# Kernel tuning notes

Hardware: AMD Instinct MI355X
Metric: run time of the kernel (lower is better)

The kernel has to match this reference:

```python
import jax, jax.numpy as jnp
import numpy as np

R, K, H_IN, W_IN = 512, 17, 56, 56   # rois, keypoints, heatmap size
ROI_H = ROI_W = 96                   # = ceil(BOX_LEN), fixed by construction
BOX_LEN = 95.5                       # all boxes have this side length
A = -0.75                            # PyTorch bicubic coefficient


def _cubic(x):
    x = jnp.abs(x)
    near = ((A + 2.0) * x - (A + 3.0)) * x * x + 1.0
    far = A * (((x - 5.0) * x + 8.0) * x - 4.0)
    return jnp.where(x <= 1.0, near, jnp.where(x < 2.0, far, 0.0))


def _resize_matrix(out_size, in_size):
    """Dense [out,in] bicubic interpolation matrix (align_corners=False, border-replicate)."""
    scale = in_size / out_size
    src = (jnp.arange(out_size, dtype=jnp.float32) + 0.5) * scale - 0.5
    base = jnp.floor(src).astype(jnp.int32)
    taps = base[:, None] + jnp.arange(-1, 3)                      # [out, 4]
    w = _cubic(src[:, None] - taps.astype(jnp.float32))           # weights from unclamped dist
    taps = jnp.clip(taps, 0, in_size - 1)                         # replicate border
    rows = jnp.broadcast_to(jnp.arange(out_size)[:, None], taps.shape)
    return jnp.zeros((out_size, in_size), jnp.float32).at[rows, taps].add(w)


def setup_inputs() -> dict:
    key = jax.random.key(0)
    k1, k2 = jax.random.split(key)
    masks = jax.random.normal(k1, (R, K, H_IN, W_IN), dtype=jnp.float32)
    offs = jax.random.uniform(k2, (R, 2), jnp.float32, 0.0, 400.0)
    # corner format (c0_start, c1_start, c0_end, c1_end); all lengths == BOX_LEN
    boxes = jnp.concatenate([offs, offs + BOX_LEN], axis=1)
    return {"masks": masks, "boxes": boxes}


def reference(masks, boxes):
    My = _resize_matrix(ROI_H, H_IN)   # [ROI_H, H_IN]
    Mx = _resize_matrix(ROI_W, W_IN)   # [ROI_W, W_IN]
    # separable bicubic resize of every ROI heatmap: [R,K,ROI_H,ROI_W]
    roi = jnp.einsum('hi,rkij,wj->rkhw', My, masks, Mx)
    flat = roi.reshape(R, K, ROI_H * ROI_W)
    pos = jnp.argmax(flat, axis=-1)                                # [R,K]
    y = pos // ROI_W
    x = pos % ROI_W
    scores = jnp.take_along_axis(flat, pos[..., None], axis=-1)[..., 0]  # logit at argmax
    len0 = jnp.maximum(boxes[:, 2] - boxes[:, 0], 1.0)
    len1 = jnp.maximum(boxes[:, 3] - boxes[:, 1], 1.0)
    corr0 = (len0 / ROI_H)[:, None]
    corr1 = (len1 / ROI_W)[:, None]
    p0 = (y.astype(jnp.float32) + 0.5) * corr0 + boxes[:, 0:1]
    p1 = (x.astype(jnp.float32) + 0.5) * corr1 + boxes[:, 1:2]
    predictions = jnp.stack([p0, p1, jnp.ones_like(p0)], axis=1)   # [R, n_dim+1, K]
    return predictions, scores
```

## Files before the change

kernel.cpp:

```cpp
#include <hip/hip_runtime.h>

#define R_    512
#define K_    17
#define HIN   56
#define WIN   56
#define OUTS  96
#define NMAP  (R_ * K_)
#define NT    64
#define GRID  (NMAP / 2)
#define WST   18
#define TROWS 60

typedef float v2f __attribute__((ext_vector_type(2)));

#define LDS_FENCE() do {                                      \
        __builtin_amdgcn_sched_barrier(0);                    \
        asm volatile("s_waitcnt lgkmcnt(0)" ::: "memory");    \
        __builtin_amdgcn_sched_barrier(0);                    \
    } while (0)

constexpr float cubic_c(float xin) {
    float x = xin < 0.0f ? -xin : xin;
    const float A = -0.75f;
    if (x <= 1.0f) return ((A + 2.0f) * x - (A + 3.0f)) * x * x + 1.0f;
    if (x < 2.0f)  return A * (((x - 5.0f) * x + 8.0f) * x - 4.0f);
    return 0.0f;
}

struct XTabT {
    float w[OUTS][4];
    int   s[OUTS];
    constexpr XTabT() : w{}, s{} {
        for (int o = 0; o < OUTS; ++o) {
            float src = ((float)o + 0.5f) * (56.0f / 96.0f) - 0.5f;
            int base = (int)src;
            if ((float)base > src) --base;
            int st = base - 1;
            if (st < 0) st = 0;
            if (st > HIN - 4) st = HIN - 4;
            s[o] = st;
            for (int q = 0; q < 4; ++q) {
                int tap = base - 1 + q;
                float wt = cubic_c(src - (float)tap);
                int p = tap < 0 ? 0 : (tap > HIN - 1 ? HIN - 1 : tap);
                w[o][p - st] += wt;
            }
        }
    }
};
constexpr XTabT XT;

struct YTabT {
    float w[12][4];
    int   d[12];
    constexpr YTabT() : w{}, d{} {
        for (int ph = 0; ph < 12; ++ph) {
            float src = ((float)ph + 0.5f) * (56.0f / 96.0f) - 0.5f;
            int base = (int)src;
            if ((float)base > src) --base;
            d[ph] = base - 1;
            for (int q = 0; q < 4; ++q)
                w[ph][q] = cubic_c(src - (float)(base - 1 + q));
        }
    }
};
constexpr YTabT YT;

template<int G> struct FSv {
    static constexpr int v = (G == 0) ? 0 : (G == 1) ? 1 : (G == 2) ? 4
                           : (G == 3) ? 6 : (G == 4) ? 8 : 10;
};

__device__ __forceinline__ v2f yv(const v2f* c, int hh) {
    const int ph = hh % 12, bb = hh / 12;
    const int i0 = 7 * bb + YT.d[ph] + 2;
    v2f acc = c[i0] * (v2f){YT.w[ph][0], YT.w[ph][0]};
    acc = __builtin_elementwise_fma((v2f){YT.w[ph][1], YT.w[ph][1]}, c[i0 + 1], acc);
    acc = __builtin_elementwise_fma((v2f){YT.w[ph][2], YT.w[ph][2]}, c[i0 + 2], acc);
    acc = __builtin_elementwise_fma((v2f){YT.w[ph][3], YT.w[ph][3]}, c[i0 + 3], acc);
    return acc;
}

template<int G>
__device__ __forceinline__ void strip_comp(float4 a0, float4 a1, float4 a2, float4 a3,
                                           float4 b0, float4 b1, float4 b2, float4 b3,
                                           v2f* wrow,
                                           const v2f* crd,
                                           int pbase,
                                           float& m0, int& p0, float& m1, int& p1) {
    constexpr int FS = FSv<G>::v;
    v2f rr[16];
    rr[0]  = (v2f){a0.x, b0.x}; rr[1]  = (v2f){a0.y, b0.y};
    rr[2]  = (v2f){a0.z, b0.z}; rr[3]  = (v2f){a0.w, b0.w};
    rr[4]  = (v2f){a1.x, b1.x}; rr[5]  = (v2f){a1.y, b1.y};
    rr[6]  = (v2f){a1.z, b1.z}; rr[7]  = (v2f){a1.w, b1.w};
    rr[8]  = (v2f){a2.x, b2.x}; rr[9]  = (v2f){a2.y, b2.y};
    rr[10] = (v2f){a2.z, b2.z}; rr[11] = (v2f){a2.w, b2.w};
    rr[12] = (v2f){a3.x, b3.x}; rr[13] = (v2f){a3.y, b3.y};
    rr[14] = (v2f){a3.z, b3.z}; rr[15] = (v2f){a3.w, b3.w};

    LDS_FENCE();
#pragma unroll
    for (int i = 0; i < 8; ++i) {
        const int o0 = 16 * G + 2 * i, o1 = o0 + 1;
        const int s0 = XT.s[o0] - 4 * FS, s1 = XT.s[o1] - 4 * FS;
        v2f x0 = rr[s0] * (v2f){XT.w[o0][0], XT.w[o0][0]};
        x0 = __builtin_elementwise_fma((v2f){XT.w[o0][1], XT.w[o0][1]}, rr[s0 + 1], x0);
        x0 = __builtin_elementwise_fma((v2f){XT.w[o0][2], XT.w[o0][2]}, rr[s0 + 2], x0);
        x0 = __builtin_elementwise_fma((v2f){XT.w[o0][3], XT.w[o0][3]}, rr[s0 + 3], x0);
        v2f x1 = rr[s1] * (v2f){XT.w[o1][0], XT.w[o1][0]};
        x1 = __builtin_elementwise_fma((v2f){XT.w[o1][1], XT.w[o1][1]}, rr[s1 + 1], x1);
        x1 = __builtin_elementwise_fma((v2f){XT.w[o1][2], XT.w[o1][2]}, rr[s1 + 2], x1);
        x1 = __builtin_elementwise_fma((v2f){XT.w[o1][3], XT.w[o1][3]}, rr[s1 + 3], x1);
        float4 st = {x0.x, x0.y, x1.x, x1.y};
        *(float4*)(wrow + 2 * i) = st;
    }
    LDS_FENCE();

    v2f c[18];
#pragma unroll
    for (int i = 0; i < 18; ++i) c[i] = crd[i * WST];

    v2f sv = {-INFINITY, -INFINITY};
    int h0i = 0, h1i = 0;
#pragma unroll
    for (int hh = 0; hh < 24; ++hh) {
        v2f a = yv(c, hh);
        if (a.x > sv.x) { sv.x = a.x; h0i = hh; }
        if (a.y > sv.y) { sv.y = a.y; h1i = hh; }
    }
    const int fp0 = pbase + 16 * G + h0i * 96;
    const int fp1 = pbase + 16 * G + h1i * 96;
    if (sv.x > m0 || (sv.x == m0 && fp0 < p0)) { m0 = sv.x; p0 = fp0; }
    if (sv.y > m1 || (sv.y == m1 && fp1 < p1)) { m1 = sv.y; p1 = fp1; }
}

__global__ __launch_bounds__(NT)
void _Keypointer_kernel(const float* __restrict__ masks,
                        const float* __restrict__ boxes,
                        float* __restrict__ out) {
    __shared__ __align__(16) v2f tmp[TROWS * WST];

    const int w   = threadIdx.x;
    const int bm0 = 2 * blockIdx.x;

    const int srcrow = min(max(w - 2, 0), HIN - 1);
    const int phys   = min(w, TROWS - 1);
    const float* r0 = masks + (size_t)bm0 * (HIN * WIN) + srcrow * WIN;
    const float* r1 = r0 + HIN * WIN;
    v2f* wrow = tmp + phys * WST;

    const int cc = w & 15, q = w >> 4;
    const v2f* crd = tmp + (14 * q) * WST + cc;
    const int pbase = (24 * q) * OUTS + cc;

    float m0 = -INFINITY, m1 = -INFINITY;
    int   p0 = 0x7fffffff, p1 = 0x7fffffff;

    float4 A0, A1, A2, A3, B0, B1, B2, B3;
    float4 C0, C1, C2, C3, D0, D1, D2, D3;

#define LOADS(FS_, X0, X1, X2, X3, Y0, Y1, Y2, Y3) {            \
        const float4* _A = (const float4*)r0 + (FS_);           \
        const float4* _B = (const float4*)r1 + (FS_);           \
        X0 = _A[0]; X1 = _A[1]; X2 = _A[2]; X3 = _A[3];         \
        Y0 = _B[0]; Y1 = _B[1]; Y2 = _B[2]; Y3 = _B[3]; }

    LOADS(0,  A0, A1, A2, A3, B0, B1, B2, B3)
    LOADS(1,  C0, C1, C2, C3, D0, D1, D2, D3)
    strip_comp<0>(A0, A1, A2, A3, B0, B1, B2, B3, wrow, crd, pbase, m0, p0, m1, p1);
    LOADS(4,  A0, A1, A2, A3, B0, B1, B2, B3)
    strip_comp<1>(C0, C1, C2, C3, D0, D1, D2, D3, wrow, crd, pbase, m0, p0, m1, p1);
    LOADS(6,  C0, C1, C2, C3, D0, D1, D2, D3)
    strip_comp<2>(A0, A1, A2, A3, B0, B1, B2, B3, wrow, crd, pbase, m0, p0, m1, p1);
    LOADS(8,  A0, A1, A2, A3, B0, B1, B2, B3)
    strip_comp<3>(C0, C1, C2, C3, D0, D1, D2, D3, wrow, crd, pbase, m0, p0, m1, p1);
    LOADS(10, C0, C1, C2, C3, D0, D1, D2, D3)
    strip_comp<4>(A0, A1, A2, A3, B0, B1, B2, B3, wrow, crd, pbase, m0, p0, m1, p1);
    strip_comp<5>(C0, C1, C2, C3, D0, D1, D2, D3, wrow, crd, pbase, m0, p0, m1, p1);
#undef LOADS

#pragma unroll
    for (int off = 32; off; off >>= 1) {
        float t0 = __shfl_xor(m0, off, 64); int u0 = __shfl_xor(p0, off, 64);
        if (t0 > m0 || (t0 == m0 && u0 < p0)) { m0 = t0; p0 = u0; }
        float t1 = __shfl_xor(m1, off, 64); int u1 = __shfl_xor(p1, off, 64);
        if (t1 > m1 || (t1 == m1 && u1 < p1)) { m1 = t1; p1 = u1; }
    }

    if (w == 0) {
#pragma unroll
        for (int mi = 0; mi < 2; ++mi) {
            const int map = bm0 + mi;
            const float M = mi ? m1 : m0;
            const int bp  = mi ? p1 : p0;
            const int r = map / K_, k = map - r * K_;
            const int y = bp / OUTS, x = bp - y * OUTS;
            const float b0f = boxes[r * 4 + 0], b1f = boxes[r * 4 + 1];
            const float b2f = boxes[r * 4 + 2], b3f = boxes[r * 4 + 3];
            const float corr0 = fmaxf(b2f - b0f, 1.0f) / (float)OUTS;
            const float corr1 = fmaxf(b3f - b1f, 1.0f) / (float)OUTS;
            const float pp0 = ((float)y + 0.5f) * corr0 + b0f;
            const float pp1 = ((float)x + 0.5f) * corr1 + b1f;
            out[(r * 3 + 0) * K_ + k] = pp0;
            out[(r * 3 + 1) * K_ + k] = pp1;
            out[(r * 3 + 2) * K_ + k] = 1.0f;
            out[R_ * 3 * K_ + r * K_ + k] = M;
        }
    }
}

extern "C" void kernel_launch(void* const* d_in, const int* in_sizes, int n_in,
                              void* d_out, int out_size, void* d_ws, size_t ws_size,
                              hipStream_t stream) {
    const float* masks = (const float*)d_in[0];
    const float* boxes = (const float*)d_in[1];
    float* out = (float*)d_out;
    _Keypointer_kernel<<<GRID, NT, 0, stream>>>(masks, boxes, out);
}
```

Measured before the change: 180.8 us.

## Restructure into persistent 384-thread blocks with LDS-staged, double-buffered map pairs

The kernel moves from one 64-thread wave per map pair to persistent 384-thread blocks that each handle four map pairs. Each pair's raw inputs are loaded with coalesced float4 reads and staged in LDS, and the next pair is prefetched into registers while the current one is computed. The six waves split the horizontal pass by column strip and the vertical pass by output column, then combine their argmax results through shared memory. This aims to improve load coalescing and hide global latency, at the cost of more LDS, extra __syncthreads, and fewer, larger blocks.

```diff
diff --git a/kernel.cpp b/kernel.cpp
--- a/kernel.cpp
+++ b/kernel.cpp
@@ -6,18 +6,15 @@
 #define WIN   56
 #define OUTS  96
 #define NMAP  (R_ * K_)
-#define NT    64
-#define GRID  (NMAP / 2)
-#define WST   18
+#define NT    384
+#define GRID  1088
+#define ITERS 4
+#define RST   98
 #define TROWS 60
+#define RAWST 58
+#define RAWMAP (HIN * RAWST)
 
 typedef float v2f __attribute__((ext_vector_type(2)));
-
-#define LDS_FENCE() do {                                      \
-        __builtin_amdgcn_sched_barrier(0);                    \
-        asm volatile("s_waitcnt lgkmcnt(0)" ::: "memory");    \
-        __builtin_amdgcn_sched_barrier(0);                    \
-    } while (0)
 
 constexpr float cubic_c(float xin) {
     float x = xin < 0.0f ? -xin : xin;
@@ -82,24 +79,16 @@
 }
 
 template<int G>
-__device__ __forceinline__ void strip_comp(float4 a0, float4 a1, float4 a2, float4 a3,
-                                           float4 b0, float4 b1, float4 b2, float4 b3,
-                                           v2f* wrow,
-                                           const v2f* crd,
-                                           int pbase,
-                                           float& m0, int& p0, float& m1, int& p1) {
+__device__ __forceinline__ void p1_lds(const float* rA, const float* rB, v2f* dst) {
     constexpr int FS = FSv<G>::v;
     v2f rr[16];
-    rr[0]  = (v2f){a0.x, b0.x}; rr[1]  = (v2f){a0.y, b0.y};
-    rr[2]  = (v2f){a0.z, b0.z}; rr[3]  = (v2f){a0.w, b0.w};
-    rr[4]  = (v2f){a1.x, b1.x}; rr[5]  = (v2f){a1.y, b1.y};
-    rr[6]  = (v2f){a1.z, b1.z}; rr[7]  = (v2f){a1.w, b1.w};
-    rr[8]  = (v2f){a2.x, b2.x}; rr[9]  = (v2f){a2.y, b2.y};
-    rr[10] = (v2f){a2.z, b2.z}; rr[11] = (v2f){a2.w, b2.w};
-    rr[12] = (v2f){a3.x, b3.x}; rr[13] = (v2f){a3.y, b3.y};
-    rr[14] = (v2f){a3.z, b3.z}; rr[15] = (v2f){a3.w, b3.w};
-
-    LDS_FENCE();
+#pragma unroll
+    for (int k = 0; k < 8; ++k) {
+        v2f a = *(const v2f*)(rA + 4 * FS + 2 * k);
+        v2f b = *(const v2f*)(rB + 4 * FS + 2 * k);
+        rr[2 * k]     = (v2f){a.x, b.x};
+        rr[2 * k + 1] = (v2f){a.y, b.y};
+    }
 #pragma unroll
     for (int i = 0; i < 8; ++i) {
         const int o0 = 16 * G + 2 * i, o1 = o0 + 1;
@@ -113,101 +102,125 @@
         x1 = __builtin_elementwise_fma((v2f){XT.w[o1][2], XT.w[o1][2]}, rr[s1 + 2], x1);
         x1 = __builtin_elementwise_fma((v2f){XT.w[o1][3], XT.w[o1][3]}, rr[s1 + 3], x1);
         float4 st = {x0.x, x0.y, x1.x, x1.y};
-        *(float4*)(wrow + 2 * i) = st;
-    }
-    LDS_FENCE();
-
-    v2f c[18];
-#pragma unroll
-    for (int i = 0; i < 18; ++i) c[i] = crd[i * WST];
-
-    v2f sv = {-INFINITY, -INFINITY};
-    int h0i = 0, h1i = 0;
-#pragma unroll
-    for (int hh = 0; hh < 24; ++hh) {
-        v2f a = yv(c, hh);
-        if (a.x > sv.x) { sv.x = a.x; h0i = hh; }
-        if (a.y > sv.y) { sv.y = a.y; h1i = hh; }
-    }
-    const int fp0 = pbase + 16 * G + h0i * 96;
-    const int fp1 = pbase + 16 * G + h1i * 96;
-    if (sv.x > m0 || (sv.x == m0 && fp0 < p0)) { m0 = sv.x; p0 = fp0; }
-    if (sv.y > m1 || (sv.y == m1 && fp1 < p1)) { m1 = sv.y; p1 = fp1; }
-}
-
-__global__ __launch_bounds__(NT)
+        *(float4*)(dst + 2 * i) = st;
+    }
+}
+
+__global__ __launch_bounds__(NT, 3)
 void _Keypointer_kernel(const float* __restrict__ masks,
                         const float* __restrict__ boxes,
                         float* __restrict__ out) {
-    __shared__ __align__(16) v2f tmp[TROWS * WST];
-
-    const int w   = threadIdx.x;
-    const int bm0 = 2 * blockIdx.x;
+    __shared__ float raw[2 * RAWMAP];
+    __shared__ __align__(16) v2f tmp[TROWS * RST];
+    __shared__ v2f wvmax[6];
+    __shared__ int wppos[6][2];
+
+    const int t = threadIdx.x;
+    const int g = t >> 6;
+    const int w = t & 63;
+
+    int off0, off1, off2, off3, off4;
+#define MKOFF(f_, dst_) { const int f = (f_); const int mp = (f >= 784);          \
+        const int rem = f - 784 * mp; const int row = rem / 14;                   \
+        const int c4 = rem - 14 * row; dst_ = mp * RAWMAP + row * RAWST + 4 * c4; }
+    MKOFF(t,        off0) MKOFF(t + 384,  off1)
+    MKOFF(t + 768,  off2) MKOFF(t + 1152, off3)
+    MKOFF(1536 + (t & 31), off4)
+#undef MKOFF
 
     const int srcrow = min(max(w - 2, 0), HIN - 1);
     const int phys   = min(w, TROWS - 1);
-    const float* r0 = masks + (size_t)bm0 * (HIN * WIN) + srcrow * WIN;
-    const float* r1 = r0 + HIN * WIN;
-    v2f* wrow = tmp + phys * WST;
-
-    const int cc = w & 15, q = w >> 4;
-    const v2f* crd = tmp + (14 * q) * WST + cc;
-    const int pbase = (24 * q) * OUTS + cc;
-
-    float m0 = -INFINITY, m1 = -INFINITY;
-    int   p0 = 0x7fffffff, p1 = 0x7fffffff;
-
-    float4 A0, A1, A2, A3, B0, B1, B2, B3;
-    float4 C0, C1, C2, C3, D0, D1, D2, D3;
-
-#define LOADS(FS_, X0, X1, X2, X3, Y0, Y1, Y2, Y3) {            \
-        const float4* _A = (const float4*)r0 + (FS_);           \
-        const float4* _B = (const float4*)r1 + (FS_);           \
-        X0 = _A[0]; X1 = _A[1]; X2 = _A[2]; X3 = _A[3];         \
-        Y0 = _B[0]; Y1 = _B[1]; Y2 = _B[2]; Y3 = _B[3]; }
-
-    LOADS(0,  A0, A1, A2, A3, B0, B1, B2, B3)
-    LOADS(1,  C0, C1, C2, C3, D0, D1, D2, D3)
-    strip_comp<0>(A0, A1, A2, A3, B0, B1, B2, B3, wrow, crd, pbase, m0, p0, m1, p1);
-    LOADS(4,  A0, A1, A2, A3, B0, B1, B2, B3)
-    strip_comp<1>(C0, C1, C2, C3, D0, D1, D2, D3, wrow, crd, pbase, m0, p0, m1, p1);
-    LOADS(6,  C0, C1, C2, C3, D0, D1, D2, D3)
-    strip_comp<2>(A0, A1, A2, A3, B0, B1, B2, B3, wrow, crd, pbase, m0, p0, m1, p1);
-    LOADS(8,  A0, A1, A2, A3, B0, B1, B2, B3)
-    strip_comp<3>(C0, C1, C2, C3, D0, D1, D2, D3, wrow, crd, pbase, m0, p0, m1, p1);
-    LOADS(10, C0, C1, C2, C3, D0, D1, D2, D3)
-    strip_comp<4>(A0, A1, A2, A3, B0, B1, B2, B3, wrow, crd, pbase, m0, p0, m1, p1);
-    strip_comp<5>(C0, C1, C2, C3, D0, D1, D2, D3, wrow, crd, pbase, m0, p0, m1, p1);
-#undef LOADS
-
-#pragma unroll
-    for (int off = 32; off; off >>= 1) {
-        float t0 = __shfl_xor(m0, off, 64); int u0 = __shfl_xor(p0, off, 64);
-        if (t0 > m0 || (t0 == m0 && u0 < p0)) { m0 = t0; p0 = u0; }
-        float t1 = __shfl_xor(m1, off, 64); int u1 = __shfl_xor(p1, off, 64);
-        if (t1 > m1 || (t1 == m1 && u1 < p1)) { m1 = t1; p1 = u1; }
-    }
-
-    if (w == 0) {
-#pragma unroll
-        for (int mi = 0; mi < 2; ++mi) {
-            const int map = bm0 + mi;
-            const float M = mi ? m1 : m0;
-            const int bp  = mi ? p1 : p0;
+    v2f* dst = tmp + phys * RST + 16 * g;
+    const float* rA = raw + srcrow * RAWST;
+    const float* rB = rA + RAWMAP;
+
+    const int q   = t / 96;
+    const int col = t - 96 * q;
+    const int h0  = 24 * q;
+    const v2f* crd = tmp + (14 * q) * RST + col;
+
+    float4 V0, V1, V2, V3, V4;
+
+    int pair = blockIdx.x;
+
+#define LOADP(p_) { const float4* gs = (const float4*)(masks + (size_t)(2 * (p_)) * (HIN * WIN)); \
+        V0 = gs[t]; V1 = gs[t + 384]; V2 = gs[t + 768]; V3 = gs[t + 1152];                        \
+        if (t < 32) V4 = gs[1536 + t]; }
+#define STAGE() { *(v2f*)(raw + off0) = (v2f){V0.x, V0.y}; *(v2f*)(raw + off0 + 2) = (v2f){V0.z, V0.w}; \
+        *(v2f*)(raw + off1) = (v2f){V1.x, V1.y}; *(v2f*)(raw + off1 + 2) = (v2f){V1.z, V1.w};           \
+        *(v2f*)(raw + off2) = (v2f){V2.x, V2.y}; *(v2f*)(raw + off2 + 2) = (v2f){V2.z, V2.w};           \
+        *(v2f*)(raw + off3) = (v2f){V3.x, V3.y}; *(v2f*)(raw + off3 + 2) = (v2f){V3.z, V3.w};           \
+        if (t < 32) { *(v2f*)(raw + off4) = (v2f){V4.x, V4.y}; *(v2f*)(raw + off4 + 2) = (v2f){V4.z, V4.w}; } }
+
+    LOADP(pair)
+    STAGE()
+    __syncthreads();
+
+    for (int it = 0; it < ITERS; ++it) {
+        const int bm0 = 2 * pair;
+        const bool more = (it + 1 < ITERS);
+
+        if (more) LOADP(pair + GRID)
+
+        if      (g == 0) p1_lds<0>(rA, rB, dst);
+        else if (g == 1) p1_lds<1>(rA, rB, dst);
+        else if (g == 2) p1_lds<2>(rA, rB, dst);
+        else if (g == 3) p1_lds<3>(rA, rB, dst);
+        else if (g == 4) p1_lds<4>(rA, rB, dst);
+        else             p1_lds<5>(rA, rB, dst);
+        __syncthreads();
+
+        if (more) STAGE()
+
+        v2f c[18];
+#pragma unroll
+        for (int i = 0; i < 18; ++i) c[i] = crd[i * RST];
+
+        v2f sv = {-INFINITY, -INFINITY};
+        int h0i = 0, h1i = 0;
+#pragma unroll
+        for (int hh = 0; hh < 24; ++hh) {
+            v2f a = yv(c, hh);
+            if (a.x > sv.x) { sv.x = a.x; h0i = hh; }
+            if (a.y > sv.y) { sv.y = a.y; h1i = hh; }
+        }
+        float m0 = sv.x, m1 = sv.y;
+        int p0 = (h0 + h0i) * OUTS + col;
+        int p1 = (h0 + h1i) * OUTS + col;
+
+#pragma unroll
+        for (int off = 32; off; off >>= 1) {
+            float t0 = __shfl_xor(m0, off, 64); int u0 = __shfl_xor(p0, off, 64);
+            if (t0 > m0 || (t0 == m0 && u0 < p0)) { m0 = t0; p0 = u0; }
+            float t1 = __shfl_xor(m1, off, 64); int u1 = __shfl_xor(p1, off, 64);
+            if (t1 > m1 || (t1 == m1 && u1 < p1)) { m1 = t1; p1 = u1; }
+        }
+        if (w == 0) { wvmax[g] = (v2f){m0, m1}; wppos[g][0] = p0; wppos[g][1] = p1; }
+        __syncthreads();
+        if (t < 2) {
+            float M = -INFINITY; int P = 0x7fffffff;
+#pragma unroll
+            for (int j = 0; j < 6; ++j) {
+                const float v = t ? wvmax[j].y : wvmax[j].x;
+                const int  pp = wppos[j][t];
+                if (v > M || (v == M && pp < P)) { M = v; P = pp; }
+            }
+            const int map = bm0 + t;
             const int r = map / K_, k = map - r * K_;
-            const int y = bp / OUTS, x = bp - y * OUTS;
+            const int y = P / OUTS, x = P - y * OUTS;
             const float b0f = boxes[r * 4 + 0], b1f = boxes[r * 4 + 1];
             const float b2f = boxes[r * 4 + 2], b3f = boxes[r * 4 + 3];
             const float corr0 = fmaxf(b2f - b0f, 1.0f) / (float)OUTS;
             const float corr1 = fmaxf(b3f - b1f, 1.0f) / (float)OUTS;
-            const float pp0 = ((float)y + 0.5f) * corr0 + b0f;
-            const float pp1 = ((float)x + 0.5f) * corr1 + b1f;
-            out[(r * 3 + 0) * K_ + k] = pp0;
-            out[(r * 3 + 1) * K_ + k] = pp1;
+            out[(r * 3 + 0) * K_ + k] = ((float)y + 0.5f) * corr0 + b0f;
+            out[(r * 3 + 1) * K_ + k] = ((float)x + 0.5f) * corr1 + b1f;
             out[(r * 3 + 2) * K_ + k] = 1.0f;
             out[R_ * 3 * K_ + r * K_ + k] = M;
         }
-    }
+        pair += GRID;
+    }
+#undef LOADP
+#undef STAGE
 }
 
 extern "C" void kernel_launch(void* const* d_in, const int* in_sizes, int n_in,
```

After: 202.2 us. +11.9%, slower.

## Stage both input heatmaps into LDS with coalesced loads before strip compute

Applied to the files above, without the earlier changes.

Replaces per-thread strided row loads from global memory, which were software-pipelined across strips, with one up-front coalesced float4 copy of both 56x56 maps into a padded LDS buffer (row stride 58). Each strip then reads its 16 columns from LDS. The aim is better global coalescing and fewer outstanding row-wise loads. In exchange it adds about 25 KB of LDS per block, which may reduce occupancy, and it gives up the overlap between loads and compute.

```diff
diff --git a/kernel.cpp b/kernel.cpp
--- a/kernel.cpp
+++ b/kernel.cpp
@@ -10,6 +10,8 @@
 #define GRID  (NMAP / 2)
 #define WST   18
 #define TROWS 60
+#define RAWST 58
+#define RAWMAP (HIN * RAWST)
 
 typedef float v2f __attribute__((ext_vector_type(2)));
 
@@ -82,24 +84,24 @@
 }
 
 template<int G>
-__device__ __forceinline__ void strip_comp(float4 a0, float4 a1, float4 a2, float4 a3,
-                                           float4 b0, float4 b1, float4 b2, float4 b3,
+__device__ __forceinline__ void strip_comp(const float* rA,
+                                           const float* rB,
                                            v2f* wrow,
                                            const v2f* crd,
                                            int pbase,
                                            float& m0, int& p0, float& m1, int& p1) {
     constexpr int FS = FSv<G>::v;
+
+    LDS_FENCE();
+
     v2f rr[16];
-    rr[0]  = (v2f){a0.x, b0.x}; rr[1]  = (v2f){a0.y, b0.y};
-    rr[2]  = (v2f){a0.z, b0.z}; rr[3]  = (v2f){a0.w, b0.w};
-    rr[4]  = (v2f){a1.x, b1.x}; rr[5]  = (v2f){a1.y, b1.y};
-    rr[6]  = (v2f){a1.z, b1.z}; rr[7]  = (v2f){a1.w, b1.w};
-    rr[8]  = (v2f){a2.x, b2.x}; rr[9]  = (v2f){a2.y, b2.y};
-    rr[10] = (v2f){a2.z, b2.z}; rr[11] = (v2f){a2.w, b2.w};
-    rr[12] = (v2f){a3.x, b3.x}; rr[13] = (v2f){a3.y, b3.y};
-    rr[14] = (v2f){a3.z, b3.z}; rr[15] = (v2f){a3.w, b3.w};
-
-    LDS_FENCE();
+#pragma unroll
+    for (int k = 0; k < 8; ++k) {
+        v2f a = *(const v2f*)(rA + 4 * FS + 2 * k);
+        v2f b = *(const v2f*)(rB + 4 * FS + 2 * k);
+        rr[2 * k]     = (v2f){a.x, b.x};
+        rr[2 * k + 1] = (v2f){a.y, b.y};
+    }
 #pragma unroll
     for (int i = 0; i < 8; ++i) {
         const int o0 = 16 * G + 2 * i, o1 = o0 + 1;
@@ -139,15 +141,42 @@
 void _Keypointer_kernel(const float* __restrict__ masks,
                         const float* __restrict__ boxes,
                         float* __restrict__ out) {
+    __shared__ float raw[2 * RAWMAP];
     __shared__ __align__(16) v2f tmp[TROWS * WST];
 
     const int w   = threadIdx.x;
     const int bm0 = 2 * blockIdx.x;
 
+    {
+        const float4* gs = (const float4*)(masks + (size_t)bm0 * (HIN * WIN));
+        float4 v[25];
+        int ofs[25];
+#pragma unroll
+        for (int j = 0; j < 25; ++j) {
+            const int f = w + 64 * j;
+            if (j < 24 || w < 32) {
+                v[j] = gs[f];
+                const int mp  = (f >= 784) ? 1 : 0;
+                const int rem = f - 784 * mp;
+                const int row = rem / 14;
+                const int c4  = rem - 14 * row;
+                ofs[j] = mp * RAWMAP + row * RAWST + 4 * c4;
+            }
+        }
+#pragma unroll
+        for (int j = 0; j < 25; ++j) {
+            if (j < 24 || w < 32) {
+                *(v2f*)(raw + ofs[j])     = (v2f){v[j].x, v[j].y};
+                *(v2f*)(raw + ofs[j] + 2) = (v2f){v[j].z, v[j].w};
+            }
+        }
+    }
+    LDS_FENCE();
+
     const int srcrow = min(max(w - 2, 0), HIN - 1);
     const int phys   = min(w, TROWS - 1);
-    const float* r0 = masks + (size_t)bm0 * (HIN * WIN) + srcrow * WIN;
-    const float* r1 = r0 + HIN * WIN;
+    const float* rA = raw + srcrow * RAWST;
+    const float* rB = rA + RAWMAP;
     v2f* wrow = tmp + phys * WST;
 
     const int cc = w & 15, q = w >> 4;
@@ -157,28 +186,12 @@
     float m0 = -INFINITY, m1 = -INFINITY;
     int   p0 = 0x7fffffff, p1 = 0x7fffffff;
 
-    float4 A0, A1, A2, A3, B0, B1, B2, B3;
-    float4 C0, C1, C2, C3, D0, D1, D2, D3;
-
-#define LOADS(FS_, X0, X1, X2, X3, Y0, Y1, Y2, Y3) {            \
-        const float4* _A = (const float4*)r0 + (FS_);           \
-        const float4* _B = (const float4*)r1 + (FS_);           \
-        X0 = _A[0]; X1 = _A[1]; X2 = _A[2]; X3 = _A[3];         \
-        Y0 = _B[0]; Y1 = _B[1]; Y2 = _B[2]; Y3 = _B[3]; }
-
-    LOADS(0,  A0, A1, A2, A3, B0, B1, B2, B3)
-    LOADS(1,  C0, C1, C2, C3, D0, D1, D2, D3)
-    strip_comp<0>(A0, A1, A2, A3, B0, B1, B2, B3, wrow, crd, pbase, m0, p0, m1, p1);
-    LOADS(4,  A0, A1, A2, A3, B0, B1, B2, B3)
-    strip_comp<1>(C0, C1, C2, C3, D0, D1, D2, D3, wrow, crd, pbase, m0, p0, m1, p1);
-    LOADS(6,  C0, C1, C2, C3, D0, D1, D2, D3)
-    strip_comp<2>(A0, A1, A2, A3, B0, B1, B2, B3, wrow, crd, pbase, m0, p0, m1, p1);
-    LOADS(8,  A0, A1, A2, A3, B0, B1, B2, B3)
-    strip_comp<3>(C0, C1, C2, C3, D0, D1, D2, D3, wrow, crd, pbase, m0, p0, m1, p1);
-    LOADS(10, C0, C1, C2, C3, D0, D1, D2, D3)
-    strip_comp<4>(A0, A1, A2, A3, B0, B1, B2, B3, wrow, crd, pbase, m0, p0, m1, p1);
-    strip_comp<5>(C0, C1, C2, C3, D0, D1, D2, D3, wrow, crd, pbase, m0, p0, m1, p1);
-#undef LOADS
+    strip_comp<0>(rA, rB, wrow, crd, pbase, m0, p0, m1, p1);
+    strip_comp<1>(rA, rB, wrow, crd, pbase, m0, p0, m1, p1);
+    strip_comp<2>(rA, rB, wrow, crd, pbase, m0, p0, m1, p1);
+    strip_comp<3>(rA, rB, wrow, crd, pbase, m0, p0, m1, p1);
+    strip_comp<4>(rA, rB, wrow, crd, pbase, m0, p0, m1, p1);
+    strip_comp<5>(rA, rB, wrow, crd, pbase, m0, p0, m1, p1);
 
 #pragma unroll
     for (int off = 32; off; off >>= 1) {
@@ -200,10 +213,8 @@
             const float b2f = boxes[r * 4 + 2], b3f = boxes[r * 4 + 3];
             const float corr0 = fmaxf(b2f - b0f, 1.0f) / (float)OUTS;
             const float corr1 = fmaxf(b3f - b1f, 1.0f) / (float)OUTS;
-            const float pp0 = ((float)y + 0.5f) * corr0 + b0f;
-            const float pp1 = ((float)x + 0.5f) * corr1 + b1f;
-            out[(r * 3 + 0) * K_ + k] = pp0;
-            out[(r * 3 + 1) * K_ + k] = pp1;
+            out[(r * 3 + 0) * K_ + k] = ((float)y + 0.5f) * corr0 + b0f;
+            out[(r * 3 + 1) * K_ + k] = ((float)x + 0.5f) * corr1 + b1f;
             out[(r * 3 + 2) * K_ + k] = 1.0f;
             out[R_ * 3 * K_ + r * K_ + k] = M;
         }
```

New measurement: 185.7 us. 2.8% more time.
